# Kernel optimization log

Measured on AMD Instinct MI355X. Metric: run time of the kernel, lower is better.

Reference implementation:

```python
import jax, jax.numpy as jnp
import numpy as np

B, NQ, C, NH, NP = 4, 16384, 256, 8, 4
HH, WW = 128, 128
HD = C // NH


def setup_inputs() -> dict:
    key = jax.random.key(0)
    ks = jax.random.split(key, 10)
    s = 1.0 / np.sqrt(C)
    return {
        'query': jax.random.normal(ks[0], (B, NQ, C), jnp.float32),
        'reference_points': jax.random.uniform(ks[1], (B, NQ, 2), jnp.float32),
        'value': jax.random.normal(ks[2], (B, HH * WW, C), jnp.float32),
        'W_off': (jax.random.normal(ks[3], (C, NH * NP * 2), jnp.float32) * 0.01),
        'b_off': (jax.random.normal(ks[4], (NH * NP * 2,), jnp.float32) * 0.5),
        'W_attn': (jax.random.normal(ks[5], (C, NH * NP), jnp.float32) * s),
        'b_attn': jnp.zeros((NH * NP,), jnp.float32),
        'W_v': (jax.random.normal(ks[6], (C, C), jnp.float32) * s),
        'b_v': jnp.zeros((C,), jnp.float32),
        'W_out': (jax.random.normal(ks[7], (C, C), jnp.float32) * s),
        'b_out': jnp.zeros((C,), jnp.float32),
        'H': HH,
        'Wd': WW,
    }


def _deform_attn(query, reference_points, value, W_off, b_off, W_attn, b_attn,
                 W_v, b_v, W_out, b_out, H, W):
    Bb, Nq, Cc = query.shape
    dt = query.dtype
    # sampling offsets [B,Nq,NH,NP,2] and softmax attention weights [B,Nq,NH,NP]
    offsets = (query @ W_off + b_off).reshape(Bb, Nq, NH, NP, 2)
    attn = jax.nn.softmax((query @ W_attn + b_attn).reshape(Bb, Nq, NH, NP), axis=-1)
    offsets = offsets / jnp.array([W, H], dt) * jnp.asarray(0.1, dt)
    loc = jnp.clip(reference_points[:, :, None, None, :] + offsets, 0.0, 1.0)
    # value projection -> per-head spatial maps, flattened HW: [B,NH,H*W,HD]
    v = (value @ W_v + b_v).reshape(Bb, H, W, NH, HD)
    v = v.transpose(0, 3, 1, 2, 4).reshape(Bb, NH, H * W, HD)
    # grid_sample bilinear, align_corners=False, zero padding:
    # grid g = loc*2-1 ; pixel = ((g+1)*size - 1)/2 = loc*size - 0.5
    ix = loc[..., 0] * W - 0.5  # [B,Nq,NH,NP]
    iy = loc[..., 1] * H - 0.5
    x0 = jnp.floor(ix); y0 = jnp.floor(iy)
    wx = ix - x0; wy = iy - y0
    x0i = x0.astype(jnp.int32); y0i = y0.astype(jnp.int32)

    def corner(xc, yc, w):
        inb = ((xc >= 0) & (xc < W) & (yc >= 0) & (yc < H)).astype(dt)
        idx = jnp.clip(yc, 0, H - 1) * W + jnp.clip(xc, 0, W - 1)  # [B,Nq,NH,NP]
        idx = idx.transpose(0, 2, 1, 3).reshape(Bb, NH, Nq * NP)
        g = jnp.take_along_axis(v, idx[..., None], axis=2)  # [B,NH,Nq*NP,HD]
        g = g.reshape(Bb, NH, Nq, NP, HD)
        return g * (w * inb).transpose(0, 2, 1, 3)[..., None]

    one = jnp.asarray(1.0, dt)
    samp = (corner(x0i, y0i, (one - wx) * (one - wy))
            + corner(x0i + 1, y0i, wx * (one - wy))
            + corner(x0i, y0i + 1, (one - wx) * wy)
            + corner(x0i + 1, y0i + 1, wx * wy))  # [B,NH,Nq,NP,HD]
    # weighted sum over points, concat heads -> [B,Nq,C]
    out = jnp.einsum('bhnpd,bnhp->bnhd', samp, attn).reshape(Bb, Nq, Cc)
    return out @ W_out + b_out


def reference(query, reference_points, value, W_off, b_off, W_attn, b_attn,
              W_v, b_v, W_out, b_out, H, Wd):
    return _deform_attn(query, reference_points, value, W_off, b_off, W_attn,
                        b_attn, W_v, b_v, W_out, b_out, H, Wd)
```

## Files before the change

kernel.cpp:

```cpp
#include <hip/hip_runtime.h>
#include <hip/hip_bf16.h>

#define HWPIX  16384
#define MTOT   65536

typedef __attribute__((ext_vector_type(8))) __bf16 bf16x8;
typedef __attribute__((ext_vector_type(4))) __bf16 bf16x4;
typedef __attribute__((ext_vector_type(4))) float  f32x4;

#define GLOAD_LDS16(gsrc, ldst)                                                  \
    __builtin_amdgcn_global_load_lds(                                            \
        (const __attribute__((address_space(1))) void*)(gsrc),                   \
        (__attribute__((address_space(3))) void*)(ldst), 16, 0, 0)

__global__ void prep_weights(const float* __restrict__ Woff,
                             const float* __restrict__ Wattn,
                             const float* __restrict__ boff,
                             const float* __restrict__ battn,
                             const float* __restrict__ Wv,
                             const float* __restrict__ Wout,
                             __bf16* __restrict__ W1t,
                             __bf16* __restrict__ Wvt,
                             __bf16* __restrict__ Wot,
                             float* __restrict__ bias1)
{
    int tid = blockIdx.x * blockDim.x + threadIdx.x;
    int stride = gridDim.x * blockDim.x;
    for (int i = tid; i < 96 * 256; i += stride) {
        int n = i >> 8, k = i & 255;
        float v = (n < 64) ? Woff[k * 64 + n] : Wattn[k * 32 + (n - 64)];
        W1t[i] = (__bf16)v;
    }
    for (int i = tid; i < 256 * 256; i += stride) {
        int n = i >> 8, k = i & 255;
        Wvt[i] = (__bf16)Wv[k * 256 + n];
        Wot[i] = (__bf16)Wout[k * 256 + n];
    }
    for (int i = tid; i < 96; i += stride)
        bias1[i] = (i < 64) ? boff[i] : battn[i - 64];
}

__global__ __launch_bounds__(256, 4) void gemm96(
    const float* __restrict__ A,
    const __bf16* __restrict__ Bt,
    const float* __restrict__ bias,
    __bf16* __restrict__ P)
{
    constexpr int NF = 6;
    __shared__ __bf16 As[2][128 * 32];
    __shared__ __bf16 Bs[2][96 * 32];

    const int tid  = threadIdx.x;
    const int wave = tid >> 6, lane = tid & 63;
    const int r16  = lane & 15, kq = lane >> 4;
    const long mbase = (long)blockIdx.x * 128;

    const float* ap0 = A + (mbase + ((tid + 0 * 256) >> 3)) * 256 + (tid & 7) * 4;
    const float* ap1 = A + (mbase + ((tid + 1 * 256) >> 3)) * 256 + (tid & 7) * 4;
    const float* ap2 = A + (mbase + ((tid + 2 * 256) >> 3)) * 256 + (tid & 7) * 4;
    const float* ap3 = A + (mbase + ((tid + 3 * 256) >> 3)) * 256 + (tid & 7) * 4;
    const __bf16* bp0 = Bt + (long)(tid >> 2) * 256 + (tid & 3) * 8;
    const __bf16* bp1 = Bt + (long)((tid + 256) >> 2) * 256 + (tid & 3) * 8;

    f32x4 acc[2][NF];
#pragma unroll
    for (int m = 0; m < 2; ++m)
#pragma unroll
        for (int n = 0; n < NF; ++n) acc[m][n] = f32x4{0.f, 0.f, 0.f, 0.f};

    float4 ra0 = *(const float4*)ap0, ra1 = *(const float4*)ap1;
    float4 ra2 = *(const float4*)ap2, ra3 = *(const float4*)ap3;
    GLOAD_LDS16(bp0, &Bs[0][tid * 8]);
    if (tid < 128) GLOAD_LDS16(bp1, &Bs[0][(tid + 256) * 8]);
#define CW96(buf)                                                                 \
    {                                                                             \
        bf16x4 o;                                                                 \
        o[0] = (__bf16)ra0.x; o[1] = (__bf16)ra0.y; o[2] = (__bf16)ra0.z; o[3] = (__bf16)ra0.w; \
        *(bf16x4*)&As[buf][(tid + 0 * 256) * 4] = o;                              \
        o[0] = (__bf16)ra1.x; o[1] = (__bf16)ra1.y; o[2] = (__bf16)ra1.z; o[3] = (__bf16)ra1.w; \
        *(bf16x4*)&As[buf][(tid + 1 * 256) * 4] = o;                              \
        o[0] = (__bf16)ra2.x; o[1] = (__bf16)ra2.y; o[2] = (__bf16)ra2.z; o[3] = (__bf16)ra2.w; \
        *(bf16x4*)&As[buf][(tid + 2 * 256) * 4] = o;                              \
        o[0] = (__bf16)ra3.x; o[1] = (__bf16)ra3.y; o[2] = (__bf16)ra3.z; o[3] = (__bf16)ra3.w; \
        *(bf16x4*)&As[buf][(tid + 3 * 256) * 4] = o;                              \
    }
    CW96(0);
    __syncthreads();

    for (int t = 0; t < 8; ++t) {
        const int cur = t & 1, nxt = cur ^ 1;
        if (t < 7) {
            const int kt = (t + 1) * 32;
            ra0 = *(const float4*)(ap0 + kt);
            ra1 = *(const float4*)(ap1 + kt);
            ra2 = *(const float4*)(ap2 + kt);
            ra3 = *(const float4*)(ap3 + kt);
            GLOAD_LDS16(bp0 + kt, &Bs[nxt][tid * 8]);
            if (tid < 128) GLOAD_LDS16(bp1 + kt, &Bs[nxt][(tid + 256) * 8]);
        }
        bf16x8 aF0 = *(const bf16x8*)&As[cur][(wave * 32 + r16) * 32 + kq * 8];
        bf16x8 aF1 = *(const bf16x8*)&As[cur][(wave * 32 + 16 + r16) * 32 + kq * 8];
#pragma unroll
        for (int n = 0; n < NF; ++n) {
            bf16x8 bF = *(const bf16x8*)&Bs[cur][(n * 16 + r16) * 32 + kq * 8];
            acc[0][n] = __builtin_amdgcn_mfma_f32_16x16x32_bf16(aF0, bF, acc[0][n], 0, 0, 0);
            acc[1][n] = __builtin_amdgcn_mfma_f32_16x16x32_bf16(aF1, bF, acc[1][n], 0, 0, 0);
        }
        if (t < 7) CW96(nxt);
        __syncthreads();
    }

#pragma unroll
    for (int m = 0; m < 2; ++m) {
        long row0 = mbase + wave * 32 + m * 16 + kq * 4;
#pragma unroll
        for (int n = 0; n < NF; ++n) {
            int col = n * 16 + r16;
            float bz = bias[col];
#pragma unroll
            for (int r = 0; r < 4; ++r)
                P[(row0 + r) * 96 + col] = (__bf16)(acc[m][n][r] + bz);
        }
    }
}

__global__ __launch_bounds__(512, 4) void gemm256_v(
    const float* __restrict__ A,
    const __bf16* __restrict__ Bt,
    const float* __restrict__ bias,
    __bf16* __restrict__ Out)
{
    __shared__ __bf16 As[2][128 * 32];
    __shared__ __bf16 Bs[2][256 * 32];

    const int tid  = threadIdx.x;
    const int wave = tid >> 6, lane = tid & 63;
    const int r16  = lane & 15, kq = lane >> 4;
    const long mbase = (long)blockIdx.x * 128;

    const float* ap0 = A + (mbase + (tid >> 3)) * 256 + (tid & 7) * 4;
    const float* ap1 = ap0 + 64 * 256;
    const __bf16* bp0 = Bt + (long)(tid >> 2) * 256 + (tid & 3) * 8;
    const __bf16* bp1 = bp0 + 128 * 256;

    f32x4 acc[16];
#pragma unroll
    for (int n = 0; n < 16; ++n) acc[n] = f32x4{0.f, 0.f, 0.f, 0.f};

    float4 ra0 = *(const float4*)ap0, ra1 = *(const float4*)ap1;
    GLOAD_LDS16(bp0, &Bs[0][tid * 8]);
    GLOAD_LDS16(bp1, &Bs[0][(tid + 512) * 8]);
#define CW256(buf)                                                                \
    {                                                                             \
        bf16x4 o;                                                                 \
        o[0] = (__bf16)ra0.x; o[1] = (__bf16)ra0.y; o[2] = (__bf16)ra0.z; o[3] = (__bf16)ra0.w; \
        *(bf16x4*)&As[buf][tid * 4] = o;                                          \
        o[0] = (__bf16)ra1.x; o[1] = (__bf16)ra1.y; o[2] = (__bf16)ra1.z; o[3] = (__bf16)ra1.w; \
        *(bf16x4*)&As[buf][(tid + 512) * 4] = o;                                  \
    }
    CW256(0);
    __syncthreads();

    for (int t = 0; t < 8; ++t) {
        const int cur = t & 1, nxt = cur ^ 1;
        if (t < 7) {
            const int kt = (t + 1) * 32;
            ra0 = *(const float4*)(ap0 + kt);
            ra1 = *(const float4*)(ap1 + kt);
            GLOAD_LDS16(bp0 + kt, &Bs[nxt][tid * 8]);
            GLOAD_LDS16(bp1 + kt, &Bs[nxt][(tid + 512) * 8]);
        }
        bf16x8 aF = *(const bf16x8*)&As[cur][(wave * 16 + r16) * 32 + kq * 8];
#pragma unroll
        for (int n = 0; n < 16; ++n) {
            bf16x8 bF = *(const bf16x8*)&Bs[cur][(n * 16 + r16) * 32 + kq * 8];
            acc[n] = __builtin_amdgcn_mfma_f32_16x16x32_bf16(aF, bF, acc[n], 0, 0, 0);
        }
        if (t < 7) CW256(nxt);
        __syncthreads();
    }

    long row0 = mbase + wave * 16 + kq * 4;
#pragma unroll
    for (int n = 0; n < 16; ++n) {
        int col = n * 16 + r16;
        float bz = bias[col];
#pragma unroll
        for (int r = 0; r < 4; ++r)
            Out[(row0 + r) * 256 + col] = (__bf16)(acc[n][r] + bz);
    }
}

#define MAKESET(E, PK)                                                            \
    {                                                                             \
        const long q_ = qbase + g * 8 + a + E;                                    \
        const __bf16* Pr_ = P + q_ * 96;                                          \
        bf16x8 off8_ = *(const bf16x8*)(Pr_ + hh * 8);                            \
        bf16x4 lg4_  = *(const bf16x4*)(Pr_ + 64 + hh * 4);                       \
        const float rx_ = refp[q_ * 2 + 0];                                       \
        const float ry_ = refp[q_ * 2 + 1];                                       \
        float lg0 = (float)lg4_[0], lg1 = (float)lg4_[1];                         \
        float lg2 = (float)lg4_[2], lg3 = (float)lg4_[3];                         \
        float mx = fmaxf(fmaxf(lg0, lg1), fmaxf(lg2, lg3));                       \
        float e0 = __expf(lg0 - mx), e1 = __expf(lg1 - mx);                       \
        float e2 = __expf(lg2 - mx), e3 = __expf(lg3 - mx);                       \
        float inv = 1.f / (e0 + e1 + e2 + e3);                                    \
        float at_[4] = {e0 * inv, e1 * inv, e2 * inv, e3 * inv};                  \
        float wxp[4], wyp[4];                                                     \
        int x0p[4], y0p[4];                                                       \
        int xmin = 127, ymin = 127;                                               \
        _Pragma("unroll")                                                         \
        for (int p = 0; p < 4; ++p) {                                             \
            float ox = (float)off8_[2 * p + 0] * (0.1f / 128.f);                  \
            float oy = (float)off8_[2 * p + 1] * (0.1f / 128.f);                  \
            float lx = fminf(fmaxf(rx_ + ox, 0.f), 1.f);                          \
            float ly = fminf(fmaxf(ry_ + oy, 0.f), 1.f);                          \
            float ixf = lx * 128.f - 0.5f;                                        \
            float iyf = ly * 128.f - 0.5f;                                        \
            float xf = floorf(ixf), yf = floorf(iyf);                             \
            wxp[p] = ixf - xf; wyp[p] = iyf - yf;                                 \
            x0p[p] = (int)xf;  y0p[p] = (int)yf;                                  \
            xmin = min(xmin, x0p[p]); ymin = min(ymin, y0p[p]);                   \
        }                                                                         \
        float wcg[3][3] = {{0.f,0.f,0.f},{0.f,0.f,0.f},{0.f,0.f,0.f}};            \
        _Pragma("unroll")                                                         \
        for (int p = 0; p < 4; ++p) {                                             \
            int dx = min(x0p[p] - xmin, 1), dy = min(y0p[p] - ymin, 1);           \
            float wx = wxp[p], wy = wyp[p], ap_ = at_[p];                         \
            float xv0 = dx ? 0.f        : 1.f - wx;                               \
            float xv1 = dx ? 1.f - wx   : wx;                                     \
            float xv2 = dx ? wx         : 0.f;                                    \
            float yv0 = (dy ? 0.f      : 1.f - wy) * ap_;                         \
            float yv1 = (dy ? 1.f - wy : wy)       * ap_;                         \
            float yv2 = (dy ? wy       : 0.f)      * ap_;                         \
            wcg[0][0] += yv0 * xv0; wcg[0][1] += yv0 * xv1; wcg[0][2] += yv0 * xv2;\
            wcg[1][0] += yv1 * xv0; wcg[1][1] += yv1 * xv1; wcg[1][2] += yv1 * xv2;\
            wcg[2][0] += yv2 * xv0; wcg[2][1] += yv2 * xv1; wcg[2][2] += yv2 * xv2;\
        }                                                                         \
        _Pragma("unroll")                                                         \
        for (int r = 0; r < 3; ++r)                                               \
            _Pragma("unroll")                                                     \
            for (int s = 0; s < 3; ++s) {                                         \
                int py = ymin + r, px = xmin + s;                                 \
                bool inb = (px >= 0) & (px < 128) & (py >= 0) & (py < 128);       \
                int pyc = min(max(py, 0), 127), pxc = min(max(px, 0), 127);       \
                float wv_ = inb ? wcg[r][s] : 0.f;                                \
                __bf16 bw_ = (__bf16)wv_;                                         \
                unsigned short wb_; __builtin_memcpy(&wb_, &bw_, 2);              \
                PK[r * 3 + s] = ((unsigned)wb_ << 16) | (unsigned)(pyc * 128 + pxc);\
            }                                                                     \
    }

__global__ __launch_bounds__(512, 4) void sample_out_fused(
    const __bf16* __restrict__ P,
    const float* __restrict__ refp,
    const __bf16* __restrict__ vproj,
    const __bf16* __restrict__ Wot,
    const float* __restrict__ bias,
    float* __restrict__ Out)
{
    __shared__ __bf16 As[128 * 256];
    __shared__ __bf16 Bs[256 * 32];

    const int tid = threadIdx.x;
    const int bid = blockIdx.x;
    const int swz = (bid & 7) * 64 + (bid >> 3);
    const long qbase = (long)swz * 128;

    {
        const int g = tid >> 5, l = tid & 31;
        const int h = l >> 2, dg = l & 3;
        const int a = l >> 3, hh = l & 7;
        const char* vbase = (const char*)(vproj + ((qbase >> 14) << 14) * 256);
        const int chbyte = h * 64 + dg * 16;

        unsigned pkA[9], pkB[9];
        MAKESET(0, pkA);
        MAKESET(4, pkB);

#pragma unroll
        for (int i = 0; i < 8; ++i) {
            const int srcl = ((i & 3) << 3) | h;
            int   bo[9];
            float w9[9];
#pragma unroll
            for (int j = 0; j < 9; ++j) {
                unsigned pk = (i < 4) ? (unsigned)__shfl((int)pkA[j], srcl, 32)
                                      : (unsigned)__shfl((int)pkB[j], srcl, 32);
                w9[j] = __uint_as_float(pk & 0xFFFF0000u);
                bo[j] = (int)(pk & 0xFFFFu) * 512 + chbyte;
            }
            uint4 v[9];
#pragma unroll
            for (int j = 0; j < 9; ++j) v[j] = uint4{0u, 0u, 0u, 0u};
#pragma unroll
            for (int j = 0; j < 9; ++j)
                if (w9[j] != 0.f)
                    v[j] = *(const uint4*)(vbase + bo[j]);

            float2 a2[4];
#pragma unroll
            for (int k = 0; k < 4; ++k) a2[k] = float2{0.f, 0.f};
#pragma unroll
            for (int j = 0; j < 9; ++j) {
                float w = w9[j];
#pragma unroll
                for (int k = 0; k < 4; ++k) {
                    unsigned u = (&v[j].x)[k];
                    a2[k].x += w * __uint_as_float(u << 16);
                    a2[k].y += w * __uint_as_float(u & 0xFFFF0000u);
                }
            }
            bf16x8 o;
#pragma unroll
            for (int k = 0; k < 4; ++k) {
                o[2 * k + 0] = (__bf16)a2[k].x;
                o[2 * k + 1] = (__bf16)a2[k].y;
            }
            int ql = g * 8 + i;
            int byte = ql * 512 + ((l * 16) ^ ((ql & 7) << 4));
            *(bf16x8*)((char*)As + byte) = o;
        }
    }

    const int wave = tid >> 6, lane = tid & 63;
    const int r16  = lane & 15, kq = lane >> 4;
    const int arow = wave * 16 + r16;
    const int abase = arow * 512;
    const int aswz  = (arow & 7) << 4;

    f32x4 acc[16];
#pragma unroll
    for (int n = 0; n < 16; ++n) acc[n] = f32x4{0.f, 0.f, 0.f, 0.f};

    for (int kt = 0; kt < 256; kt += 32) {
        __syncthreads();
        for (int c = tid; c < 1024; c += 512)
            GLOAD_LDS16(Wot + (long)(c >> 2) * 256 + kt + (c & 3) * 8, &Bs[c * 8]);
        __syncthreads();
        bf16x8 aF = *(const bf16x8*)((char*)As + abase + ((kt * 2 + kq * 16) ^ aswz));
        __builtin_amdgcn_s_setprio(1);
#pragma unroll
        for (int n = 0; n < 16; ++n) {
            bf16x8 bF = *(const bf16x8*)&Bs[(n * 16 + r16) * 32 + kq * 8];
            acc[n] = __builtin_amdgcn_mfma_f32_16x16x32_bf16(aF, bF, acc[n], 0, 0, 0);
        }
        __builtin_amdgcn_s_setprio(0);
    }

    long row0 = qbase + wave * 16 + kq * 4;
#pragma unroll
    for (int n = 0; n < 16; ++n) {
        int col = n * 16 + r16;
        float bz = bias[col];
#pragma unroll
        for (int r = 0; r < 4; ++r)
            Out[(row0 + r) * 256 + col] = acc[n][r] + bz;
    }
}

extern "C" void kernel_launch(void* const* d_in, const int* in_sizes, int n_in,
                              void* d_out, int out_size, void* d_ws, size_t ws_size,
                              hipStream_t stream)
{
    const float* query  = (const float*)d_in[0];
    const float* refp   = (const float*)d_in[1];
    const float* value  = (const float*)d_in[2];
    const float* W_off  = (const float*)d_in[3];
    const float* b_off  = (const float*)d_in[4];
    const float* W_attn = (const float*)d_in[5];
    const float* b_attn = (const float*)d_in[6];
    const float* W_v    = (const float*)d_in[7];
    const float* b_v    = (const float*)d_in[8];
    const float* W_out  = (const float*)d_in[9];
    const float* b_out  = (const float*)d_in[10];

    char* w = (char*)d_ws;
    __bf16* P       = (__bf16*)w;  w += (size_t)MTOT * 96 * 2;
    __bf16* vproj   = (__bf16*)w;  w += (size_t)MTOT * 256 * 2;
    __bf16* W1t     = (__bf16*)w;  w += 96 * 256 * 2;
    __bf16* Wvt     = (__bf16*)w;  w += 256 * 256 * 2;
    __bf16* Wot     = (__bf16*)w;  w += 256 * 256 * 2;
    float*  bias1   = (float*)w;   w += 96 * 4;

    prep_weights<<<120, 256, 0, stream>>>(W_off, W_attn, b_off, b_attn,
                                          W_v, W_out, W1t, Wvt, Wot, bias1);
    gemm96<<<MTOT / 128, 256, 0, stream>>>(query, W1t, bias1, P);
    gemm256_v<<<MTOT / 128, 512, 0, stream>>>(value, Wvt, b_v, vproj);
    sample_out_fused<<<MTOT / 128, 512, 0, stream>>>(P, refp, vproj, Wot, b_out,
                                                     (float*)d_out);
}
```

Baseline: 77.80 us.

## Fuse offset/attention projection GEMM into the sampling-output kernel

Removes the separate gemm96 kernel and computes the query projection (offsets and attention logits) inside sample_out_fused for each 128-query tile, writing the result to shared memory instead of a global P buffer. This drops one kernel launch and the global write and read of the 96-column intermediate. In exchange the fused kernel does a single-buffered K loop with two barriers per step, reuses the LDS regions for staging, and adds an extra barrier before the sampling stage, which may lengthen the fused kernel.

```diff
diff --git a/kernel.cpp b/kernel.cpp
--- a/kernel.cpp
+++ b/kernel.cpp
@@ -40,90 +40,6 @@
         bias1[i] = (i < 64) ? boff[i] : battn[i - 64];
 }
 
-__global__ __launch_bounds__(256, 4) void gemm96(
-    const float* __restrict__ A,
-    const __bf16* __restrict__ Bt,
-    const float* __restrict__ bias,
-    __bf16* __restrict__ P)
-{
-    constexpr int NF = 6;
-    __shared__ __bf16 As[2][128 * 32];
-    __shared__ __bf16 Bs[2][96 * 32];
-
-    const int tid  = threadIdx.x;
-    const int wave = tid >> 6, lane = tid & 63;
-    const int r16  = lane & 15, kq = lane >> 4;
-    const long mbase = (long)blockIdx.x * 128;
-
-    const float* ap0 = A + (mbase + ((tid + 0 * 256) >> 3)) * 256 + (tid & 7) * 4;
-    const float* ap1 = A + (mbase + ((tid + 1 * 256) >> 3)) * 256 + (tid & 7) * 4;
-    const float* ap2 = A + (mbase + ((tid + 2 * 256) >> 3)) * 256 + (tid & 7) * 4;
-    const float* ap3 = A + (mbase + ((tid + 3 * 256) >> 3)) * 256 + (tid & 7) * 4;
-    const __bf16* bp0 = Bt + (long)(tid >> 2) * 256 + (tid & 3) * 8;
-    const __bf16* bp1 = Bt + (long)((tid + 256) >> 2) * 256 + (tid & 3) * 8;
-
-    f32x4 acc[2][NF];
-#pragma unroll
-    for (int m = 0; m < 2; ++m)
-#pragma unroll
-        for (int n = 0; n < NF; ++n) acc[m][n] = f32x4{0.f, 0.f, 0.f, 0.f};
-
-    float4 ra0 = *(const float4*)ap0, ra1 = *(const float4*)ap1;
-    float4 ra2 = *(const float4*)ap2, ra3 = *(const float4*)ap3;
-    GLOAD_LDS16(bp0, &Bs[0][tid * 8]);
-    if (tid < 128) GLOAD_LDS16(bp1, &Bs[0][(tid + 256) * 8]);
-#define CW96(buf)                                                                 \
-    {                                                                             \
-        bf16x4 o;                                                                 \
-        o[0] = (__bf16)ra0.x; o[1] = (__bf16)ra0.y; o[2] = (__bf16)ra0.z; o[3] = (__bf16)ra0.w; \
-        *(bf16x4*)&As[buf][(tid + 0 * 256) * 4] = o;                              \
-        o[0] = (__bf16)ra1.x; o[1] = (__bf16)ra1.y; o[2] = (__bf16)ra1.z; o[3] = (__bf16)ra1.w; \
-        *(bf16x4*)&As[buf][(tid + 1 * 256) * 4] = o;                              \
-        o[0] = (__bf16)ra2.x; o[1] = (__bf16)ra2.y; o[2] = (__bf16)ra2.z; o[3] = (__bf16)ra2.w; \
-        *(bf16x4*)&As[buf][(tid + 2 * 256) * 4] = o;                              \
-        o[0] = (__bf16)ra3.x; o[1] = (__bf16)ra3.y; o[2] = (__bf16)ra3.z; o[3] = (__bf16)ra3.w; \
-        *(bf16x4*)&As[buf][(tid + 3 * 256) * 4] = o;                              \
-    }
-    CW96(0);
-    __syncthreads();
-
-    for (int t = 0; t < 8; ++t) {
-        const int cur = t & 1, nxt = cur ^ 1;
-        if (t < 7) {
-            const int kt = (t + 1) * 32;
-            ra0 = *(const float4*)(ap0 + kt);
-            ra1 = *(const float4*)(ap1 + kt);
-            ra2 = *(const float4*)(ap2 + kt);
-            ra3 = *(const float4*)(ap3 + kt);
-            GLOAD_LDS16(bp0 + kt, &Bs[nxt][tid * 8]);
-            if (tid < 128) GLOAD_LDS16(bp1 + kt, &Bs[nxt][(tid + 256) * 8]);
-        }
-        bf16x8 aF0 = *(const bf16x8*)&As[cur][(wave * 32 + r16) * 32 + kq * 8];
-        bf16x8 aF1 = *(const bf16x8*)&As[cur][(wave * 32 + 16 + r16) * 32 + kq * 8];
-#pragma unroll
-        for (int n = 0; n < NF; ++n) {
-            bf16x8 bF = *(const bf16x8*)&Bs[cur][(n * 16 + r16) * 32 + kq * 8];
-            acc[0][n] = __builtin_amdgcn_mfma_f32_16x16x32_bf16(aF0, bF, acc[0][n], 0, 0, 0);
-            acc[1][n] = __builtin_amdgcn_mfma_f32_16x16x32_bf16(aF1, bF, acc[1][n], 0, 0, 0);
-        }
-        if (t < 7) CW96(nxt);
-        __syncthreads();
-    }
-
-#pragma unroll
-    for (int m = 0; m < 2; ++m) {
-        long row0 = mbase + wave * 32 + m * 16 + kq * 4;
-#pragma unroll
-        for (int n = 0; n < NF; ++n) {
-            int col = n * 16 + r16;
-            float bz = bias[col];
-#pragma unroll
-            for (int r = 0; r < 4; ++r)
-                P[(row0 + r) * 96 + col] = (__bf16)(acc[m][n][r] + bz);
-        }
-    }
-}
-
 __global__ __launch_bounds__(512, 4) void gemm256_v(
     const float* __restrict__ A,
     const __bf16* __restrict__ Bt,
@@ -191,16 +107,13 @@
     }
 }
 
-#define MAKESET(E, PK)                                                            \
+#define MAKESET(E, OFF8_, LG4_, PK)                                               \
     {                                                                             \
         const long q_ = qbase + g * 8 + a + E;                                    \
-        const __bf16* Pr_ = P + q_ * 96;                                          \
-        bf16x8 off8_ = *(const bf16x8*)(Pr_ + hh * 8);                            \
-        bf16x4 lg4_  = *(const bf16x4*)(Pr_ + 64 + hh * 4);                       \
         const float rx_ = refp[q_ * 2 + 0];                                       \
         const float ry_ = refp[q_ * 2 + 1];                                       \
-        float lg0 = (float)lg4_[0], lg1 = (float)lg4_[1];                         \
-        float lg2 = (float)lg4_[2], lg3 = (float)lg4_[3];                         \
+        float lg0 = (float)LG4_[0], lg1 = (float)LG4_[1];                         \
+        float lg2 = (float)LG4_[2], lg3 = (float)LG4_[3];                         \
         float mx = fmaxf(fmaxf(lg0, lg1), fmaxf(lg2, lg3));                       \
         float e0 = __expf(lg0 - mx), e1 = __expf(lg1 - mx);                       \
         float e2 = __expf(lg2 - mx), e3 = __expf(lg3 - mx);                       \
@@ -211,8 +124,8 @@
         int xmin = 127, ymin = 127;                                               \
         _Pragma("unroll")                                                         \
         for (int p = 0; p < 4; ++p) {                                             \
-            float ox = (float)off8_[2 * p + 0] * (0.1f / 128.f);                  \
-            float oy = (float)off8_[2 * p + 1] * (0.1f / 128.f);                  \
+            float ox = (float)OFF8_[2 * p + 0] * (0.1f / 128.f);                  \
+            float oy = (float)OFF8_[2 * p + 1] * (0.1f / 128.f);                  \
             float lx = fminf(fmaxf(rx_ + ox, 0.f), 1.f);                          \
             float ly = fminf(fmaxf(ry_ + oy, 0.f), 1.f);                          \
             float ixf = lx * 128.f - 0.5f;                                        \
@@ -252,9 +165,11 @@
     }
 
 __global__ __launch_bounds__(512, 4) void sample_out_fused(
-    const __bf16* __restrict__ P,
+    const float* __restrict__ query,
     const float* __restrict__ refp,
     const __bf16* __restrict__ vproj,
+    const __bf16* __restrict__ W1t,
+    const float* __restrict__ bias1,
     const __bf16* __restrict__ Wot,
     const float* __restrict__ bias,
     float* __restrict__ Out)
@@ -267,6 +182,52 @@
     const int swz = (bid & 7) * 64 + (bid >> 3);
     const long qbase = (long)swz * 128;
 
+    const int wave = tid >> 6, lane = tid & 63;
+    const int r16  = lane & 15, kq = lane >> 4;
+
+    __bf16* Pl = (__bf16*)((char*)As + 40960);
+
+    {
+        f32x4 pacc[6];
+#pragma unroll
+        for (int n = 0; n < 6; ++n) pacc[n] = f32x4{0.f, 0.f, 0.f, 0.f};
+
+        for (int kt = 0; kt < 256; kt += 32) {
+            __syncthreads();
+            {
+                const float4* src = (const float4*)(query +
+                    (qbase + (tid >> 2)) * 256 + kt + (tid & 3) * 8);
+                float4 v0 = src[0], v1 = src[1];
+                bf16x8 o;
+                o[0] = (__bf16)v0.x; o[1] = (__bf16)v0.y;
+                o[2] = (__bf16)v0.z; o[3] = (__bf16)v0.w;
+                o[4] = (__bf16)v1.x; o[5] = (__bf16)v1.y;
+                o[6] = (__bf16)v1.z; o[7] = (__bf16)v1.w;
+                *(bf16x8*)&Bs[tid * 8] = o;
+            }
+            if (tid < 384)
+                GLOAD_LDS16(W1t + (long)(tid >> 2) * 256 + kt + (tid & 3) * 8,
+                            &As[tid * 8]);
+            __syncthreads();
+            bf16x8 aF = *(const bf16x8*)&Bs[(wave * 16 + r16) * 32 + kq * 8];
+#pragma unroll
+            for (int n = 0; n < 6; ++n) {
+                bf16x8 bF = *(const bf16x8*)&As[(n * 16 + r16) * 32 + kq * 8];
+                pacc[n] = __builtin_amdgcn_mfma_f32_16x16x32_bf16(aF, bF, pacc[n], 0, 0, 0);
+            }
+        }
+        int prow = wave * 16 + kq * 4;
+#pragma unroll
+        for (int n = 0; n < 6; ++n) {
+            int col = n * 16 + r16;
+            float bz = bias1[col];
+#pragma unroll
+            for (int r = 0; r < 4; ++r)
+                Pl[(prow + r) * 96 + col] = (__bf16)(pacc[n][r] + bz);
+        }
+    }
+    __syncthreads();
+
     {
         const int g = tid >> 5, l = tid & 31;
         const int h = l >> 2, dg = l & 3;
@@ -274,9 +235,16 @@
         const char* vbase = (const char*)(vproj + ((qbase >> 14) << 14) * 256);
         const int chbyte = h * 64 + dg * 16;
 
+        bf16x8 off8A = *(const bf16x8*)&Pl[(g * 8 + a + 0) * 96 + hh * 8];
+        bf16x4 lg4A  = *(const bf16x4*)&Pl[(g * 8 + a + 0) * 96 + 64 + hh * 4];
+        bf16x8 off8B = *(const bf16x8*)&Pl[(g * 8 + a + 4) * 96 + hh * 8];
+        bf16x4 lg4B  = *(const bf16x4*)&Pl[(g * 8 + a + 4) * 96 + 64 + hh * 4];
+
         unsigned pkA[9], pkB[9];
-        MAKESET(0, pkA);
-        MAKESET(4, pkB);
+        MAKESET(0, off8A, lg4A, pkA);
+        MAKESET(4, off8B, lg4B, pkB);
+
+        __syncthreads();
 
 #pragma unroll
         for (int i = 0; i < 8; ++i) {
@@ -323,8 +291,6 @@
         }
     }
 
-    const int wave = tid >> 6, lane = tid & 63;
-    const int r16  = lane & 15, kq = lane >> 4;
     const int arow = wave * 16 + r16;
     const int abase = arow * 512;
     const int aswz  = (arow & 7) << 4;
@@ -376,7 +342,6 @@
     const float* b_out  = (const float*)d_in[10];
 
     char* w = (char*)d_ws;
-    __bf16* P       = (__bf16*)w;  w += (size_t)MTOT * 96 * 2;
     __bf16* vproj   = (__bf16*)w;  w += (size_t)MTOT * 256 * 2;
     __bf16* W1t     = (__bf16*)w;  w += 96 * 256 * 2;
     __bf16* Wvt     = (__bf16*)w;  w += 256 * 256 * 2;
@@ -385,8 +350,8 @@
 
     prep_weights<<<120, 256, 0, stream>>>(W_off, W_attn, b_off, b_attn,
                                           W_v, W_out, W1t, Wvt, Wot, bias1);
-    gemm96<<<MTOT / 128, 256, 0, stream>>>(query, W1t, bias1, P);
     gemm256_v<<<MTOT / 128, 512, 0, stream>>>(value, Wvt, b_v, vproj);
-    sample_out_fused<<<MTOT / 128, 512, 0, stream>>>(P, refp, vproj, Wot, b_out,
+    sample_out_fused<<<MTOT / 128, 512, 0, stream>>>(query, refp, vproj,
+                                                     W1t, bias1, Wot, b_out,
                                                      (float*)d_out);
 }
```

Result: no change. 78.20 us (+0.5%).
